# Kernel optimization log

Measured on AMD Instinct MI355X. Metric: run time of the kernel, lower is better.

Reference implementation:

```python
import jax, jax.numpy as jnp
import numpy as np

D_MODEL, D_K, D_V, H, GRID = 512, 64, 64, 8, 196
B = 4


def setup_inputs() -> dict:
    key = jax.random.key(0)
    ks = jax.random.split(key, 12)
    s = 0.02
    return {
        "queries": jax.random.normal(ks[0], (B, GRID, D_MODEL), jnp.float32),
        "keys": jax.random.normal(ks[1], (B, GRID, D_MODEL), jnp.float32),
        "values": jax.random.normal(ks[2], (B, GRID, D_MODEL), jnp.float32),
        "Wq": jax.random.normal(ks[3], (H * D_K, D_MODEL), jnp.float32) * s,
        "bq": jnp.zeros((H * D_K,), jnp.float32),
        "Wk": jax.random.normal(ks[4], (H * D_K, D_MODEL), jnp.float32) * s,
        "bk": jnp.zeros((H * D_K,), jnp.float32),
        "Wv": jax.random.normal(ks[5], (H * D_V, D_MODEL), jnp.float32) * s,
        "bv": jnp.zeros((H * D_V,), jnp.float32),
        "Wo": jax.random.normal(ks[6], (D_MODEL, H * D_V), jnp.float32) * s,
        "bo": jnp.zeros((D_MODEL,), jnp.float32),
        "scale": jnp.ones((1, H, GRID, GRID), jnp.float32) / np.sqrt(D_K).astype(np.float32),
    }


def reference(queries, keys, values, Wq, bq, Wk, bk, Wv, bv, Wo, bo, scale):
    b, nq, _ = queries.shape
    nk = values.shape[1]
    # linear projections (torch nn.Linear: x @ W.T + b)
    q_sig = queries @ Wq.T + bq          # (b, nq, h*dk)
    k_p = keys @ Wk.T + bk               # (b, nk, h*dk)
    v_p = values @ Wv.T + bv             # (b, nk, h*dv)
    # elementwise q*k interaction (b, nq, nk, h*dk)
    att_e = q_sig[:, :, None, :] * k_p[:, None, :, :]
    # sigmoid-gated values
    v_g = jax.nn.sigmoid(att_e) * v_p[:, None, :, :]
    v = v_g.reshape(b, nq, nk, H, D_K).transpose(0, 3, 1, 2, 4)      # (b,h,nq,nk,dk)
    att = att_e.reshape(b, nq, nk, H, D_K).transpose(0, 3, 1, 2, 4)  # (b,h,nq,nk,dk)
    att = att.sum(-1) * scale            # (b,h,nq,nk)
    p = jax.nn.softmax(att, axis=-1)     # dropout is identity in eval mode
    # (att.unsqueeze(-2) @ v).squeeze(-2)
    image = jnp.einsum("bhqk,bhqkd->bhqd", p, v)
    image = image.transpose(0, 2, 1, 3).reshape(b, nq, H * D_V)
    out = image @ Wo.T + bo              # (b, nq, d_model)
    out = jax.nn.sigmoid(q_sig * out) * out
    return out
```

## Files before the change

### kernel.cpp

```cpp
#include <hip/hip_runtime.h>
#include <hip/hip_bf16.h>
#include <math.h>

#define NQ 196
#define BATCH 4
#define HD 512
#define NH 8
#define DK 64
#define MROWS 784
#define MPAD 832

typedef __attribute__((ext_vector_type(8))) short short8;
typedef __attribute__((ext_vector_type(4))) short short4v;
typedef __attribute__((ext_vector_type(4))) float float4v;

__device__ __forceinline__ float b2f(short s) {
  return __uint_as_float(((unsigned)(unsigned short)s) << 16);
}
__device__ __forceinline__ short f2b(float x) {
  return __builtin_bit_cast(short, __float2bfloat16(x));
}
__device__ __forceinline__ float fexp2(float x) {
  float r; asm("v_exp_f32 %0, %1" : "=v"(r) : "v"(x)); return r;
}
__device__ __forceinline__ float frcp(float x) {
  float r; asm("v_rcp_f32 %0, %1" : "=v"(r) : "v"(x)); return r;
}
__device__ __forceinline__ void cvt4(float4 v, short4v& hi, short4v& lo) {
  float x[4] = {v.x, v.y, v.z, v.w};
  #pragma unroll
  for (int i = 0; i < 4; ++i) {
    hi[i] = f2b(x[i]);
    lo[i] = f2b(x[i] - b2f(hi[i]));
  }
}
__device__ __forceinline__ void cvt8(float4 v0, float4 v1, short8& hi, short8& lo) {
  short4v h0, l0, h1, l1;
  cvt4(v0, h0, l0); cvt4(v1, h1, l1);
  hi = short8{h0[0],h0[1],h0[2],h0[3],h1[0],h1[1],h1[2],h1[3]};
  lo = short8{l0[0],l0[1],l0[2],l0[3],l1[0],l1[1],l1[2],l1[3]};
}
__device__ __forceinline__ void gload_lds16(const void* g, void* l) {
  __builtin_amdgcn_global_load_lds(
      (const __attribute__((address_space(1))) unsigned int*)g,
      (__attribute__((address_space(3))) unsigned int*)l, 16, 0, 0);
}

struct ProjArgs {
  const float* X[3]; const float* W[3]; const float* bias[3];
  float* Cf[3]; short* Ch[3]; short* Cl[3];
  const float* Wo; short* Woh; short* Wol;
};

__global__ __launch_bounds__(512)
void proj_kernel(ProjArgs a) {
  const int z = blockIdx.z;
  const float* __restrict__ X = a.X[z];
  const float* __restrict__ W = a.W[z];
  const int t = threadIdx.x;
  const int ln = t & 63, lm = ln & 15, quad = ln >> 4;
  const int w = t >> 6, wm = w >> 1, wn = w & 1;
  const int m0 = blockIdx.x << 6, n0 = blockIdx.y << 6;

  __shared__ __align__(16) short smem[32768];

  const int sr = t >> 3;
  const int cg = (t & 7) << 3;
  const int wIdx = sr * 64 + (cg ^ ((sr & 7) << 3));
  const float* gA = X + (size_t)min(m0 + sr, MROWS - 1) * HD;
  const float* gB = W + (size_t)(n0 + sr) * HD;

  float4 ra0, ra1, rb0, rb1;
  float4v acc0 = {0.f,0.f,0.f,0.f}, acc1 = {0.f,0.f,0.f,0.f};
  const int ar = (wm << 4) + lm;
  const int br0 = (wn << 5) + lm, br1 = br0 + 16;
  const int swz = (lm & 7) << 3;

  ra0 = *(const float4*)(gA + cg);     ra1 = *(const float4*)(gA + cg + 4);
  rb0 = *(const float4*)(gB + cg);     rb1 = *(const float4*)(gB + cg + 4);
  {
    short8 hi, lo;
    cvt8(ra0, ra1, hi, lo);
    *(short8*)&smem[0    + wIdx] = hi;  *(short8*)&smem[4096  + wIdx] = lo;
    cvt8(rb0, rb1, hi, lo);
    *(short8*)&smem[8192 + wIdx] = hi;  *(short8*)&smem[12288 + wIdx] = lo;
  }

  for (int kt = 0; kt < 8; ++kt) {
    const int buf = kt & 1;
    __syncthreads();
    if (kt < 7) {
      const int kb = (kt + 1) << 6;
      ra0 = *(const float4*)(gA + kb + cg);  ra1 = *(const float4*)(gA + kb + cg + 4);
      rb0 = *(const float4*)(gB + kb + cg);  rb1 = *(const float4*)(gB + kb + cg + 4);
    }
    const short* Sb = smem + (buf << 14);
    #pragma unroll
    for (int h2 = 0; h2 < 2; ++h2) {
      const int c = (h2 << 5) + (quad << 3);
      const int cs = c ^ swz;
      short8 a_h = *(const short8*)&Sb[         ar  * 64 + cs];
      short8 a_l = *(const short8*)&Sb[4096  +  ar  * 64 + cs];
      short8 b0h = *(const short8*)&Sb[8192  +  br0 * 64 + cs];
      short8 b0l = *(const short8*)&Sb[12288 +  br0 * 64 + cs];
      short8 b1h = *(const short8*)&Sb[8192  +  br1 * 64 + cs];
      short8 b1l = *(const short8*)&Sb[12288 +  br1 * 64 + cs];
      acc0 = __builtin_amdgcn_mfma_f32_16x16x32_bf16(a_h, b0h, acc0, 0,0,0);
      acc0 = __builtin_amdgcn_mfma_f32_16x16x32_bf16(a_h, b0l, acc0, 0,0,0);
      acc0 = __builtin_amdgcn_mfma_f32_16x16x32_bf16(a_l, b0h, acc0, 0,0,0);
      acc1 = __builtin_amdgcn_mfma_f32_16x16x32_bf16(a_h, b1h, acc1, 0,0,0);
      acc1 = __builtin_amdgcn_mfma_f32_16x16x32_bf16(a_h, b1l, acc1, 0,0,0);
      acc1 = __builtin_amdgcn_mfma_f32_16x16x32_bf16(a_l, b1h, acc1, 0,0,0);
    }
    if (kt < 7) {
      short* Nb = smem + ((buf ^ 1) << 14);
      short8 hi, lo;
      cvt8(ra0, ra1, hi, lo);
      *(short8*)&Nb[0    + wIdx] = hi;  *(short8*)&Nb[4096  + wIdx] = lo;
      cvt8(rb0, rb1, hi, lo);
      *(short8*)&Nb[8192 + wIdx] = hi;  *(short8*)&Nb[12288 + wIdx] = lo;
    }
  }

  {
    const float* bias = a.bias[z];
    float* Cf = a.Cf[z]; short* Ch = a.Ch[z]; short* Cl = a.Cl[z];
    #pragma unroll
    for (int nf = 0; nf < 2; ++nf) {
      const float4v av = nf ? acc1 : acc0;
      const int n = n0 + (wn << 5) + (nf << 4) + lm;
      const float bv = bias[n];
      #pragma unroll
      for (int r = 0; r < 4; ++r) {
        const int m = m0 + (wm << 4) + (quad << 2) + r;
        const float c = av[r] + bv;
        Cf[(size_t)m * HD + n] = c;
        if (Ch) {
          const short hi = f2b(c);
          Ch[(size_t)m * HD + n] = hi;
          Cl[(size_t)m * HD + n] = f2b(c - b2f(hi));
        }
      }
    }
  }

  if (z == 2) {
    const int lin = blockIdx.y * 13 + blockIdx.x;
    if (lin < 64) {
      const size_t off = (size_t)lin * 4096 + (size_t)t * 8;
      float4 v0 = *(const float4*)(a.Wo + off);
      float4 v1 = *(const float4*)(a.Wo + off + 4);
      short8 hi, lo; cvt8(v0, v1, hi, lo);
      *(short8*)(a.Woh + off) = hi;
      *(short8*)(a.Wol + off) = lo;
    }
  }
}

__global__ __launch_bounds__(512)
void attn_fused(const short* __restrict__ qsh, const short* __restrict__ qsl,
                const short* __restrict__ ksh, const short* __restrict__ ksl,
                const float* __restrict__ qsg, const float* __restrict__ kpg,
                const float* __restrict__ vpg, const float* __restrict__ scg,
                short* __restrict__ imgh, short* __restrict__ imgl) {
  const int q0 = blockIdx.x * 16;
  const int h  = blockIdx.y;
  const int b  = blockIdx.z;
  const int t  = threadIdx.x;
  const int w = t >> 6, ln = t & 63;
  const int lm = ln & 15, quad = ln >> 4;
  const float L2E = 1.4426950408889634f;

  __shared__ __align__(16) float S[16][212];
  __shared__ float R[8][16][64];

  const size_t abase = ((size_t)(b * NQ) + q0 + lm) * HD + h * DK + (quad << 3);
  short8 ah0 = *(const short8*)(qsh + abase);
  short8 ah1 = *(const short8*)(qsh + abase + 32);
  short8 al0 = *(const short8*)(qsl + abase);
  short8 al1 = *(const short8*)(qsl + abase + 32);

  for (int nt = w; nt < 13; nt += 8) {
    const size_t bbase = ((size_t)(b * NQ) + nt * 16 + lm) * HD + h * DK + (quad << 3);
    short8 bh0 = *(const short8*)(ksh + bbase);
    short8 bh1 = *(const short8*)(ksh + bbase + 32);
    short8 bl0 = *(const short8*)(ksl + bbase);
    short8 bl1 = *(const short8*)(ksl + bbase + 32);
    float4v acc = {0.f, 0.f, 0.f, 0.f};
    acc = __builtin_amdgcn_mfma_f32_16x16x32_bf16(ah0, bh0, acc, 0,0,0);
    acc = __builtin_amdgcn_mfma_f32_16x16x32_bf16(ah1, bh1, acc, 0,0,0);
    acc = __builtin_amdgcn_mfma_f32_16x16x32_bf16(ah0, bl0, acc, 0,0,0);
    acc = __builtin_amdgcn_mfma_f32_16x16x32_bf16(ah1, bl1, acc, 0,0,0);
    acc = __builtin_amdgcn_mfma_f32_16x16x32_bf16(al0, bh0, acc, 0,0,0);
    acc = __builtin_amdgcn_mfma_f32_16x16x32_bf16(al1, bh1, acc, 0,0,0);
    #pragma unroll
    for (int r = 0; r < 4; ++r)
      S[(quad << 2) + r][nt * 16 + lm] = acc[r];
  }
  __syncthreads();

  for (int i = 0; i < 2; ++i) {
    const int rr = (w << 1) + i;
    const int q = q0 + rr;
    const bool qok = q < NQ;
    const float* srow = scg + ((size_t)h * NQ + (qok ? q : 0)) * NQ;
    float att[4];
    #pragma unroll
    for (int j = 0; j < 4; ++j) {
      const int c = ln + (j << 6);
      att[j] = -1e30f;
      if (c < NQ) att[j] = S[rr][c] * srow[c] * L2E;
    }
    float m = fmaxf(fmaxf(att[0], att[1]), fmaxf(att[2], att[3]));
    #pragma unroll
    for (int off = 32; off; off >>= 1) m = fmaxf(m, __shfl_xor(m, off, 64));
    float e[4], s = 0.f;
    #pragma unroll
    for (int j = 0; j < 4; ++j) { e[j] = fexp2(att[j] - m); s += e[j]; }
    #pragma unroll
    for (int off = 32; off; off >>= 1) s += __shfl_xor(s, off, 64);
    const float rinv = __fdividef(1.f, s);
    #pragma unroll
    for (int j = 0; j < 4; ++j) {
      const int c = ln + (j << 6);
      if (c < NQ) S[rr][c] = e[j] * rinv;
    }
  }
  __syncthreads();

  const int d = ln;
  const int kg = w;
  const int kbeg = kg * 24;
  const int kend = (kg == 7) ? 196 : kbeg + 24;
  const float LOG2E = 1.4426950408889634f;

  float nqs[16];
  #pragma unroll
  for (int qi = 0; qi < 16; ++qi) {
    const int row = min(b * NQ + q0 + qi, MROWS - 1);
    nqs[qi] = -qsg[(size_t)row * HD + h * DK + d] * LOG2E;
  }
  const float* kp = kpg + ((size_t)(b * NQ)) * HD + h * DK + d;
  const float* vp = vpg + ((size_t)(b * NQ)) * HD + h * DK + d;

  float acc[16];
  #pragma unroll
  for (int qi = 0; qi < 16; ++qi) acc[qi] = 0.f;

  for (int k = kbeg; k < kend; k += 4) {
    const float kv0 = kp[(size_t)(k + 0) * HD];
    const float kv1 = kp[(size_t)(k + 1) * HD];
    const float kv2 = kp[(size_t)(k + 2) * HD];
    const float kv3 = kp[(size_t)(k + 3) * HD];
    const float vv0 = vp[(size_t)(k + 0) * HD];
    const float vv1 = vp[(size_t)(k + 1) * HD];
    const float vv2 = vp[(size_t)(k + 2) * HD];
    const float vv3 = vp[(size_t)(k + 3) * HD];
    #pragma unroll
    for (int qi = 0; qi < 16; ++qi) {
      const float4 s4 = *(const float4*)&S[qi][k];
      acc[qi] += s4.x * (vv0 * frcp(1.f + fexp2(nqs[qi] * kv0)));
      acc[qi] += s4.y * (vv1 * frcp(1.f + fexp2(nqs[qi] * kv1)));
      acc[qi] += s4.z * (vv2 * frcp(1.f + fexp2(nqs[qi] * kv2)));
      acc[qi] += s4.w * (vv3 * frcp(1.f + fexp2(nqs[qi] * kv3)));
    }
  }
  #pragma unroll
  for (int qi = 0; qi < 16; ++qi) R[kg][qi][d] = acc[qi];
  __syncthreads();

  #pragma unroll
  for (int j = 0; j < 2; ++j) {
    const int idx = t + (j << 9);
    const int qi = idx >> 6, dd = idx & 63;
    const int q = q0 + qi;
    if (q < NQ) {
      float s = 0.f;
      #pragma unroll
      for (int kk = 0; kk < 8; ++kk) s += R[kk][qi][dd];
      const size_t o = ((size_t)(b * NQ) + q) * HD + h * DK + dd;
      const short hi = f2b(s);
      imgh[o] = hi;
      imgl[o] = f2b(s - b2f(hi));
    }
  }
}

__global__ __launch_bounds__(512)
void out_kernel(const short* __restrict__ Ahp, const short* __restrict__ Alp,
                const short* __restrict__ Bhp, const short* __restrict__ Blp,
                const float* __restrict__ bo, const float* __restrict__ q_sig,
                float* __restrict__ out) {
  __shared__ short smem[32768];
  const int t = threadIdx.x;
  const int ln = t & 63, lm = ln & 15, quad = ln >> 4;
  const int w = t >> 6;
  const int wm = w >> 1, wn = w & 1;
  const int m0 = blockIdx.x << 6, n0 = blockIdx.y << 6;

  const int sr = t >> 3;
  const int sc = ((t & 7) ^ (sr & 7)) << 3;
  const short* gA_h = Ahp + (size_t)(m0 + sr) * HD + sc;
  const short* gA_l = Alp + (size_t)(m0 + sr) * HD + sc;
  const short* gB_h = Bhp + (size_t)(n0 + sr) * HD + sc;
  const short* gB_l = Blp + (size_t)(n0 + sr) * HD + sc;
  const int ldst = t * 8;

  float4v acc0 = {0.f,0.f,0.f,0.f}, acc1 = {0.f,0.f,0.f,0.f};

  gload_lds16(gA_h, &smem[0     + ldst]);
  gload_lds16(gA_l, &smem[4096  + ldst]);
  gload_lds16(gB_h, &smem[8192  + ldst]);
  gload_lds16(gB_l, &smem[12288 + ldst]);

  const int ar = (wm << 4) + lm;
  const int br0 = (wn << 5) + lm, br1 = br0 + 16;
  const int swz = (lm & 7) << 3;

  for (int kt = 0; kt < 8; ++kt) {
    const int buf = kt & 1;
    __syncthreads();
    if (kt < 7) {
      const int kb = (kt + 1) << 6;
      short* nb = &smem[(buf ^ 1) << 14];
      gload_lds16(gA_h + kb, nb + 0     + ldst);
      gload_lds16(gA_l + kb, nb + 4096  + ldst);
      gload_lds16(gB_h + kb, nb + 8192  + ldst);
      gload_lds16(gB_l + kb, nb + 12288 + ldst);
    }
    const short* Sb = &smem[buf << 14];
    #pragma unroll
    for (int h2 = 0; h2 < 2; ++h2) {
      const int c = (h2 << 5) + (quad << 3);
      const int cs = c ^ swz;
      short8 a_h = *(const short8*)&Sb[         ar  * 64 + cs];
      short8 a_l = *(const short8*)&Sb[4096  +  ar  * 64 + cs];
      short8 b0h = *(const short8*)&Sb[8192  +  br0 * 64 + cs];
      short8 b0l = *(const short8*)&Sb[12288 +  br0 * 64 + cs];
      short8 b1h = *(const short8*)&Sb[8192  +  br1 * 64 + cs];
      short8 b1l = *(const short8*)&Sb[12288 +  br1 * 64 + cs];
      acc0 = __builtin_amdgcn_mfma_f32_16x16x32_bf16(a_h, b0h, acc0, 0,0,0);
      acc0 = __builtin_amdgcn_mfma_f32_16x16x32_bf16(a_h, b0l, acc0, 0,0,0);
      acc0 = __builtin_amdgcn_mfma_f32_16x16x32_bf16(a_l, b0h, acc0, 0,0,0);
      acc1 = __builtin_amdgcn_mfma_f32_16x16x32_bf16(a_h, b1h, acc1, 0,0,0);
      acc1 = __builtin_amdgcn_mfma_f32_16x16x32_bf16(a_h, b1l, acc1, 0,0,0);
      acc1 = __builtin_amdgcn_mfma_f32_16x16x32_bf16(a_l, b1h, acc1, 0,0,0);
    }
  }

  #pragma unroll
  for (int nf = 0; nf < 2; ++nf) {
    const float4v av = nf ? acc1 : acc0;
    const int n = n0 + (wn << 5) + (nf << 4) + lm;
    const float bv = bo[n];
    #pragma unroll
    for (int r = 0; r < 4; ++r) {
      const int m = m0 + (wm << 4) + (quad << 2) + r;
      if (m < MROWS) {
        float c = av[r] + bv;
        const float qg = q_sig[(size_t)m * HD + n];
        c = __fdividef(c, 1.f + __expf(-qg * c));
        out[(size_t)m * HD + n] = c;
      }
    }
  }
}

extern "C" void kernel_launch(void* const* d_in, const int* in_sizes, int n_in,
                              void* d_out, int out_size, void* d_ws, size_t ws_size,
                              hipStream_t stream) {
  const float* queries = (const float*)d_in[0];
  const float* keys    = (const float*)d_in[1];
  const float* values  = (const float*)d_in[2];
  const float* Wq = (const float*)d_in[3];
  const float* bq = (const float*)d_in[4];
  const float* Wk = (const float*)d_in[5];
  const float* bk = (const float*)d_in[6];
  const float* Wv = (const float*)d_in[7];
  const float* bv = (const float*)d_in[8];
  const float* Wo = (const float*)d_in[9];
  const float* bo = (const float*)d_in[10];
  const float* scale = (const float*)d_in[11];

  char* base = (char*)d_ws;
  const size_t NELPS = (size_t)MPAD * HD;
  const size_t WEL   = (size_t)HD * HD;

  size_t o = 0;
  float* q_sig = (float*)(base + o); o += NELPS * 4;
  float* k_p   = (float*)(base + o); o += NELPS * 4;
  float* v_p   = (float*)(base + o); o += NELPS * 4;
  short* qsh = (short*)(base + o); o += NELPS * 2;
  short* qsl = (short*)(base + o); o += NELPS * 2;
  short* ksh = (short*)(base + o); o += NELPS * 2;
  short* ksl = (short*)(base + o); o += NELPS * 2;
  short* imgh = (short*)(base + o); o += NELPS * 2;
  short* imgl = (short*)(base + o); o += NELPS * 2;
  short* Woh = (short*)(base + o); o += WEL * 2;
  short* Wol = (short*)(base + o); o += WEL * 2;

  ProjArgs p;
  p.X[0] = queries; p.X[1] = keys; p.X[2] = values;
  p.W[0] = Wq;      p.W[1] = Wk;   p.W[2] = Wv;
  p.bias[0] = bq;   p.bias[1] = bk; p.bias[2] = bv;
  p.Cf[0] = q_sig;  p.Cf[1] = k_p;  p.Cf[2] = v_p;
  p.Ch[0] = qsh; p.Cl[0] = qsl;
  p.Ch[1] = ksh; p.Cl[1] = ksl;
  p.Ch[2] = nullptr; p.Cl[2] = nullptr;
  p.Wo = Wo; p.Woh = Woh; p.Wol = Wol;
  proj_kernel<<<dim3(MPAD/64, HD/64, 3), 512, 0, stream>>>(p);

  attn_fused<<<dim3(13, NH, BATCH), 512, 0, stream>>>(
      qsh, qsl, ksh, ksl, q_sig, k_p, v_p, scale, imgh, imgl);

  out_kernel<<<dim3(MPAD/64, HD/64), 512, 0, stream>>>(
      imgh, imgl, Woh, Wol, bo, q_sig, (float*)d_out);
}
```

Measured before the change: 134.2 us.

## Repartition attention gating loop and halve output GEMM row tile

In the attention kernel, the gated-value accumulation now splits work across warps as 4 query rows by 2 key halves, instead of 16 query rows by 8 key chunks. This cuts per-thread accumulator registers and the final reduction to two partials, but each thread re-reads its k/v values for more key positions. The output projection kernel uses 32-row M tiles with one 16x16 accumulator per warp, doubling the block count and shrinking LDS use. This trades per-block reuse for more parallelism across CUs.

```diff
diff --git a/kernel.cpp b/kernel.cpp
--- a/kernel.cpp
+++ b/kernel.cpp
@@ -172,7 +172,7 @@
   const float L2E = 1.4426950408889634f;
 
   __shared__ __align__(16) float S[16][212];
-  __shared__ float R[8][16][64];
+  __shared__ float R2[2][16][64];
 
   const size_t abase = ((size_t)(b * NQ) + q0 + lm) * HD + h * DK + (quad << 3);
   short8 ah0 = *(const short8*)(qsh + abase);
@@ -228,45 +228,46 @@
   }
   __syncthreads();
 
-  const int d = ln;
-  const int kg = w;
-  const int kbeg = kg * 24;
-  const int kend = (kg == 7) ? 196 : kbeg + 24;
-  const float LOG2E = 1.4426950408889634f;
-
-  float nqs[16];
-  #pragma unroll
-  for (int qi = 0; qi < 16; ++qi) {
-    const int row = min(b * NQ + q0 + qi, MROWS - 1);
-    nqs[qi] = -qsg[(size_t)row * HD + h * DK + d] * LOG2E;
-  }
-  const float* kp = kpg + ((size_t)(b * NQ)) * HD + h * DK + d;
-  const float* vp = vpg + ((size_t)(b * NQ)) * HD + h * DK + d;
-
-  float acc[16];
-  #pragma unroll
-  for (int qi = 0; qi < 16; ++qi) acc[qi] = 0.f;
-
-  for (int k = kbeg; k < kend; k += 4) {
-    const float kv0 = kp[(size_t)(k + 0) * HD];
-    const float kv1 = kp[(size_t)(k + 1) * HD];
-    const float kv2 = kp[(size_t)(k + 2) * HD];
-    const float kv3 = kp[(size_t)(k + 3) * HD];
-    const float vv0 = vp[(size_t)(k + 0) * HD];
-    const float vv1 = vp[(size_t)(k + 1) * HD];
-    const float vv2 = vp[(size_t)(k + 2) * HD];
-    const float vv3 = vp[(size_t)(k + 3) * HD];
-    #pragma unroll
-    for (int qi = 0; qi < 16; ++qi) {
-      const float4 s4 = *(const float4*)&S[qi][k];
-      acc[qi] += s4.x * (vv0 * frcp(1.f + fexp2(nqs[qi] * kv0)));
-      acc[qi] += s4.y * (vv1 * frcp(1.f + fexp2(nqs[qi] * kv1)));
-      acc[qi] += s4.z * (vv2 * frcp(1.f + fexp2(nqs[qi] * kv2)));
-      acc[qi] += s4.w * (vv3 * frcp(1.f + fexp2(nqs[qi] * kv3)));
-    }
-  }
-  #pragma unroll
-  for (int qi = 0; qi < 16; ++qi) R[kg][qi][d] = acc[qi];
+  {
+    const int d = ln;
+    const int qg = (w >> 1) << 2;
+    const int kh = w & 1;
+    const int kbeg = kh ? 100 : 0;
+    const int kend = kh ? 196 : 100;
+    const float LOG2E = 1.4426950408889634f;
+
+    float nqs[4];
+    #pragma unroll
+    for (int qi = 0; qi < 4; ++qi) {
+      const int row = min(b * NQ + q0 + qg + qi, MROWS - 1);
+      nqs[qi] = -qsg[(size_t)row * HD + h * DK + d] * LOG2E;
+    }
+    const float* kp = kpg + ((size_t)(b * NQ)) * HD + h * DK + d;
+    const float* vp = vpg + ((size_t)(b * NQ)) * HD + h * DK + d;
+
+    float acc[4] = {0.f, 0.f, 0.f, 0.f};
+
+    for (int k = kbeg; k < kend; k += 4) {
+      const float kv0 = kp[(size_t)(k + 0) * HD];
+      const float kv1 = kp[(size_t)(k + 1) * HD];
+      const float kv2 = kp[(size_t)(k + 2) * HD];
+      const float kv3 = kp[(size_t)(k + 3) * HD];
+      const float vv0 = vp[(size_t)(k + 0) * HD];
+      const float vv1 = vp[(size_t)(k + 1) * HD];
+      const float vv2 = vp[(size_t)(k + 2) * HD];
+      const float vv3 = vp[(size_t)(k + 3) * HD];
+      #pragma unroll
+      for (int qi = 0; qi < 4; ++qi) {
+        const float4 s4 = *(const float4*)&S[qg + qi][k];
+        acc[qi] += s4.x * (vv0 * frcp(1.f + fexp2(nqs[qi] * kv0)));
+        acc[qi] += s4.y * (vv1 * frcp(1.f + fexp2(nqs[qi] * kv1)));
+        acc[qi] += s4.z * (vv2 * frcp(1.f + fexp2(nqs[qi] * kv2)));
+        acc[qi] += s4.w * (vv3 * frcp(1.f + fexp2(nqs[qi] * kv3)));
+      }
+    }
+    #pragma unroll
+    for (int qi = 0; qi < 4; ++qi) R2[kh][qg + qi][d] = acc[qi];
+  }
   __syncthreads();
 
   #pragma unroll
@@ -275,9 +276,7 @@
     const int qi = idx >> 6, dd = idx & 63;
     const int q = q0 + qi;
     if (q < NQ) {
-      float s = 0.f;
-      #pragma unroll
-      for (int kk = 0; kk < 8; ++kk) s += R[kk][qi][dd];
+      const float s = R2[0][qi][dd] + R2[1][qi][dd];
       const size_t o = ((size_t)(b * NQ) + q) * HD + h * DK + dd;
       const short hi = f2b(s);
       imgh[o] = hi;
@@ -291,30 +290,33 @@
                 const short* __restrict__ Bhp, const short* __restrict__ Blp,
                 const float* __restrict__ bo, const float* __restrict__ q_sig,
                 float* __restrict__ out) {
-  __shared__ short smem[32768];
+  __shared__ short smem[24576];
   const int t = threadIdx.x;
   const int ln = t & 63, lm = ln & 15, quad = ln >> 4;
   const int w = t >> 6;
-  const int wm = w >> 1, wn = w & 1;
-  const int m0 = blockIdx.x << 6, n0 = blockIdx.y << 6;
+  const int wm = w >> 2, wn = w & 3;
+  const int m0 = blockIdx.x << 5, n0 = blockIdx.y << 6;
 
   const int sr = t >> 3;
   const int sc = ((t & 7) ^ (sr & 7)) << 3;
-  const short* gA_h = Ahp + (size_t)(m0 + sr) * HD + sc;
-  const short* gA_l = Alp + (size_t)(m0 + sr) * HD + sc;
   const short* gB_h = Bhp + (size_t)(n0 + sr) * HD + sc;
   const short* gB_l = Blp + (size_t)(n0 + sr) * HD + sc;
-  const int ldst = t * 8;
-
-  float4v acc0 = {0.f,0.f,0.f,0.f}, acc1 = {0.f,0.f,0.f,0.f};
-
-  gload_lds16(gA_h, &smem[0     + ldst]);
-  gload_lds16(gA_l, &smem[4096  + ldst]);
-  gload_lds16(gB_h, &smem[8192  + ldst]);
-  gload_lds16(gB_l, &smem[12288 + ldst]);
+  const int tt = t & 255;
+  const int ra = tt >> 3;
+  const int sca = ((tt & 7) ^ (ra & 7)) << 3;
+  const short* gA = ((t < 256) ? Ahp : Alp) + (size_t)(m0 + ra) * HD + sca;
+  const int aoff = (t < 256) ? 0 : 2048;
+  const int ldstA = aoff + tt * 8;
+  const int ldstB = t * 8;
+
+  float4v acc = {0.f,0.f,0.f,0.f};
+
+  gload_lds16(gA,   &smem[ldstA]);
+  gload_lds16(gB_h, &smem[4096 + ldstB]);
+  gload_lds16(gB_l, &smem[8192 + ldstB]);
 
   const int ar = (wm << 4) + lm;
-  const int br0 = (wn << 5) + lm, br1 = br0 + 16;
+  const int br = (wn << 4) + lm;
   const int swz = (lm & 7) << 3;
 
   for (int kt = 0; kt < 8; ++kt) {
@@ -322,42 +324,34 @@
     __syncthreads();
     if (kt < 7) {
       const int kb = (kt + 1) << 6;
-      short* nb = &smem[(buf ^ 1) << 14];
-      gload_lds16(gA_h + kb, nb + 0     + ldst);
-      gload_lds16(gA_l + kb, nb + 4096  + ldst);
-      gload_lds16(gB_h + kb, nb + 8192  + ldst);
-      gload_lds16(gB_l + kb, nb + 12288 + ldst);
-    }
-    const short* Sb = &smem[buf << 14];
+      short* nb = &smem[(buf ^ 1) * 12288];
+      gload_lds16(gA + kb,   &nb[ldstA]);
+      gload_lds16(gB_h + kb, &nb[4096 + ldstB]);
+      gload_lds16(gB_l + kb, &nb[8192 + ldstB]);
+    }
+    const short* Sb = &smem[buf * 12288];
     #pragma unroll
     for (int h2 = 0; h2 < 2; ++h2) {
       const int c = (h2 << 5) + (quad << 3);
       const int cs = c ^ swz;
-      short8 a_h = *(const short8*)&Sb[         ar  * 64 + cs];
-      short8 a_l = *(const short8*)&Sb[4096  +  ar  * 64 + cs];
-      short8 b0h = *(const short8*)&Sb[8192  +  br0 * 64 + cs];
-      short8 b0l = *(const short8*)&Sb[12288 +  br0 * 64 + cs];
-      short8 b1h = *(const short8*)&Sb[8192  +  br1 * 64 + cs];
-      short8 b1l = *(const short8*)&Sb[12288 +  br1 * 64 + cs];
-      acc0 = __builtin_amdgcn_mfma_f32_16x16x32_bf16(a_h, b0h, acc0, 0,0,0);
-      acc0 = __builtin_amdgcn_mfma_f32_16x16x32_bf16(a_h, b0l, acc0, 0,0,0);
-      acc0 = __builtin_amdgcn_mfma_f32_16x16x32_bf16(a_l, b0h, acc0, 0,0,0);
-      acc1 = __builtin_amdgcn_mfma_f32_16x16x32_bf16(a_h, b1h, acc1, 0,0,0);
-      acc1 = __builtin_amdgcn_mfma_f32_16x16x32_bf16(a_h, b1l, acc1, 0,0,0);
-      acc1 = __builtin_amdgcn_mfma_f32_16x16x32_bf16(a_l, b1h, acc1, 0,0,0);
-    }
-  }
-
-  #pragma unroll
-  for (int nf = 0; nf < 2; ++nf) {
-    const float4v av = nf ? acc1 : acc0;
-    const int n = n0 + (wn << 5) + (nf << 4) + lm;
+      short8 a_h = *(const short8*)&Sb[         ar * 64 + cs];
+      short8 a_l = *(const short8*)&Sb[2048  +  ar * 64 + cs];
+      short8 b_h = *(const short8*)&Sb[4096  +  br * 64 + cs];
+      short8 b_l = *(const short8*)&Sb[8192  +  br * 64 + cs];
+      acc = __builtin_amdgcn_mfma_f32_16x16x32_bf16(a_h, b_h, acc, 0,0,0);
+      acc = __builtin_amdgcn_mfma_f32_16x16x32_bf16(a_h, b_l, acc, 0,0,0);
+      acc = __builtin_amdgcn_mfma_f32_16x16x32_bf16(a_l, b_h, acc, 0,0,0);
+    }
+  }
+
+  {
+    const int n = n0 + (wn << 4) + lm;
     const float bv = bo[n];
     #pragma unroll
     for (int r = 0; r < 4; ++r) {
       const int m = m0 + (wm << 4) + (quad << 2) + r;
       if (m < MROWS) {
-        float c = av[r] + bv;
+        float c = acc[r] + bv;
         const float qg = q_sig[(size_t)m * HD + n];
         c = __fdividef(c, 1.f + __expf(-qg * c));
         out[(size_t)m * HD + n] = c;
@@ -413,6 +407,6 @@
   attn_fused<<<dim3(13, NH, BATCH), 512, 0, stream>>>(
       qsh, qsl, ksh, ksl, q_sig, k_p, v_p, scale, imgh, imgl);
 
-  out_kernel<<<dim3(MPAD/64, HD/64), 512, 0, stream>>>(
+  out_kernel<<<dim3(MPAD/32, HD/64), 512, 0, stream>>>(
       imgh, imgl, Woh, Wol, bo, q_sig, (float*)d_out);
 }
```

New measurement: 131.2 us. 2.3% less time.
